# Optimization experiments

Hardware: AMD Instinct MI355X
Metric: run time of the kernel (lower is better)

Reference implementation:

```python
import jax, jax.numpy as jnp
import numpy as np

N_NODES = 100000
N_EDGES = 3200000
N_FEAT = 512
N_DIMS = 64
N_CLSS = 10


def setup_inputs() -> dict:
    key = jax.random.key(0)
    ks = jax.random.split(key, 8)
    x = jax.random.normal(ks[0], (N_NODES, N_FEAT), dtype=jnp.float32)
    edge_index = jax.random.randint(ks[1], (2, N_EDGES), 0, N_NODES, dtype=jnp.int64)
    edge_weight = jax.random.uniform(ks[2], (N_EDGES,), dtype=jnp.float32)
    W1 = jax.random.normal(ks[3], (N_FEAT, N_DIMS), dtype=jnp.float32) * (1.0 / np.sqrt(N_FEAT))
    M1 = jax.random.normal(ks[4], (N_FEAT, N_DIMS), dtype=jnp.float32)
    b1 = jnp.zeros((N_DIMS,), dtype=jnp.float32)
    W2 = jax.random.normal(ks[5], (N_DIMS, N_CLSS), dtype=jnp.float32) * (1.0 / np.sqrt(N_DIMS))
    M2 = jax.random.normal(ks[6], (N_DIMS, N_CLSS), dtype=jnp.float32)
    b2 = jnp.zeros((N_CLSS,), dtype=jnp.float32)
    return {"x": x, "edge_index": edge_index, "edge_weight": edge_weight,
            "W1": W1, "M1": M1, "b1": b1, "W2": W2, "M2": M2, "b2": b2}


def _gcn_conv(x, edge_index, edge_weight, W, M, b):
    # MaskedGCNConv: weight = W * mask, then standard GCN symmetric-normalized propagation.
    N = x.shape[0]
    h = x @ (W * M)  # [N, n_dims]  transform-first (in_feat > out_feat)
    # add self-loops with weight 1 (GCNConv default)
    loop = jnp.arange(N, dtype=edge_index.dtype)
    src = jnp.concatenate([edge_index[0], loop])
    dst = jnp.concatenate([edge_index[1], loop])
    w = jnp.concatenate([edge_weight, jnp.ones((N,), dtype=edge_weight.dtype)])
    deg = jax.ops.segment_sum(w, dst, num_segments=N)  # in-degree with weights
    deg_inv_sqrt = jnp.where(deg > 0, jax.lax.rsqrt(jnp.maximum(deg, 1e-12)), 0.0)
    norm = deg_inv_sqrt[src] * w * deg_inv_sqrt[dst]  # [E+N]
    out = jax.ops.segment_sum(h[src] * norm[:, None], dst, num_segments=N)
    return out + b


def reference(x, edge_index, edge_weight, W1, M1, b1, W2, M2, b2):
    h = jax.nn.relu(_gcn_conv(x, edge_index, edge_weight, W1, M1, b1))
    # F.dropout(training=self.training): identity in eval mode
    logits = h @ (W2 * M2) + b2  # MaskedLinear classifier
    return logits
```

## Files before the change

### kernel.cpp

```cpp
#include <hip/hip_runtime.h>

#define NN 100000
#define NE 3200000
#define NF 512
#define ND 64
#define NC 10
#define NB 391

#define OFF_H      0
#define OFF_RANK   0
#define OFF_DIS    6400000
#define OFF_W1     6500000
#define OFF_CNT    6533408
#define OFF_RP     6633408
#define OFF_BSUM   6733409
#define OFF_EDGE   6733922
#define OFF_W2F    13133922

typedef __attribute__((ext_vector_type(8))) short v8s;
typedef __attribute__((ext_vector_type(4))) float v4f;

__device__ __forceinline__ unsigned short bf16_rne(float f) {
  unsigned int u = __float_as_uint(f);
  return (unsigned short)((u + 0x7fffu + ((u >> 16) & 1u)) >> 16);
}

__global__ __launch_bounds__(256) void prep_kernel(
    const float* __restrict__ W1, const float* __restrict__ M1,
    const float* __restrict__ W2, const float* __restrict__ M2,
    float* __restrict__ ws) {
  const int i = blockIdx.x * 256 + threadIdx.x;
  if (i < NN) ((int*)ws)[OFF_CNT + i] = 0;
  if (i < NF * ND) {
    const float v = W1[i] * M1[i];
    const int k = i >> 6, d = i & 63;
    const int s = k >> 5, g = (k >> 3) & 3, e = k & 7;
    const int t = d >> 4;
    const int lane = (g << 4) | (d & 15);
    unsigned short* bp = (unsigned short*)(ws + OFF_W1);
    const int base = ((s * 4 + t) * 64 + lane) * 16 + e;
    const unsigned short hb = bf16_rne(v);
    bp[base] = hb;
    bp[base + 8] = bf16_rne(v - __uint_as_float((unsigned int)hb << 16));
  }
  if (i < ND * 16) {
    const int k = i >> 4, c = i & 15;
    const float v = (c < NC) ? W2[k * NC + c] * M2[k * NC + c] : 0.0f;
    const int s = k >> 5, g = (k >> 3) & 3, e = k & 7;
    const int lane = (g << 4) | c;
    unsigned short* bp = (unsigned short*)(ws + OFF_W2F);
    const int base = (s * 64 + lane) * 16 + e;
    const unsigned short hb = bf16_rne(v);
    bp[base] = hb;
    bp[base + 8] = bf16_rne(v - __uint_as_float((unsigned int)hb << 16));
  }
}

__global__ __launch_bounds__(256) void hist_kernel(
    const int* __restrict__ dst, int* __restrict__ cnt,
    int* __restrict__ rank) {
  const int e = blockIdx.x * 256 + threadIdx.x;
  rank[e] = atomicAdd(&cnt[dst[e]], 1);
}

__global__ __launch_bounds__(256) void scan_partial(
    const int* __restrict__ cnt, int* __restrict__ bsum) {
  __shared__ int s[256];
  const int i = blockIdx.x * 256 + threadIdx.x;
  int v = (i < NN) ? cnt[i] : 0;
  s[threadIdx.x] = v; __syncthreads();
  for (int off = 128; off > 0; off >>= 1) {
    if (threadIdx.x < off) s[threadIdx.x] += s[threadIdx.x + off];
    __syncthreads();
  }
  if (threadIdx.x == 0) bsum[blockIdx.x] = s[0];
}

__global__ __launch_bounds__(512) void scan_bsum(int* __restrict__ bsum) {
  __shared__ int s[512];
  const int t = threadIdx.x;
  const int v = (t < NB) ? bsum[t] : 0;
  s[t] = v; __syncthreads();
  for (int off = 1; off < 512; off <<= 1) {
    const int a = (t >= off) ? s[t - off] : 0;
    __syncthreads();
    s[t] += a;
    __syncthreads();
  }
  if (t < NB) bsum[t] = s[t] - v;
}

__global__ __launch_bounds__(256) void scan_final(
    const int* __restrict__ cnt, const int* __restrict__ bsum,
    int* __restrict__ rowptr) {
  __shared__ int s[256];
  const int i = blockIdx.x * 256 + threadIdx.x;
  const int v = (i < NN) ? cnt[i] : 0;
  s[threadIdx.x] = v; __syncthreads();
  for (int off = 1; off < 256; off <<= 1) {
    const int a = (threadIdx.x >= off) ? s[threadIdx.x - off] : 0;
    __syncthreads();
    s[threadIdx.x] += a;
    __syncthreads();
  }
  if (i < NN) {
    const int excl = s[threadIdx.x] - v + bsum[blockIdx.x];
    rowptr[i] = excl;
    if (i == NN - 1) rowptr[NN] = excl + v;
  }
}

__global__ __launch_bounds__(256) void fill_kernel(
    const int* __restrict__ src, const int* __restrict__ dst,
    const float* __restrict__ ew, const int* __restrict__ rank,
    const int* __restrict__ rowptr, int2* __restrict__ edge) {
  const int e = blockIdx.x * 256 + threadIdx.x;
  const int pos = rowptr[dst[e]] + rank[e];
  edge[pos] = make_int2(src[e], __float_as_int(ew[e]));
}

__global__ __launch_bounds__(256) void degdis_kernel(
    const int* __restrict__ rowptr, const int2* __restrict__ edge,
    float* __restrict__ dis) {
  const int n = blockIdx.x * 256 + threadIdx.x;
  if (n >= NN) return;
  const int beg = rowptr[n], end = rowptr[n + 1];
  float s = 1.0f;
  for (int e = beg; e < end; ++e) s += __int_as_float(edge[e].y);
  dis[n] = rsqrtf(s);
}

__global__ __launch_bounds__(256) void gemm1_kernel(
    const float* __restrict__ x, const float* __restrict__ bfrag_f,
    const float* __restrict__ dis, float* __restrict__ h) {
  const int lane = threadIdx.x & 63;
  const int wid  = threadIdx.x >> 6;
  const size_t row0 = ((size_t)blockIdx.x * 4 + wid) * 32;
  if (row0 >= NN) return;
  const int lr = lane & 15;
  const int lg = lane >> 4;
  const float* x0 = x + (row0 + lr) * NF + lg * 8;
  const v8s* bfr = (const v8s*)bfrag_f + (size_t)lane * 2;
  v4f acc[2][4];
#pragma unroll
  for (int i = 0; i < 2; ++i)
#pragma unroll
    for (int t = 0; t < 4; ++t) acc[i][t] = (v4f){0.f, 0.f, 0.f, 0.f};

  for (int s = 0; s < 16; ++s) {
    v8s ah[2], al[2];
#pragma unroll
    for (int i = 0; i < 2; ++i) {
      const float* xp = x0 + (size_t)i * (16 * NF) + s * 32;
      const float4 p0 = *(const float4*)xp;
      const float4 p1 = *(const float4*)(xp + 4);
      const float vv[8] = {p0.x, p0.y, p0.z, p0.w, p1.x, p1.y, p1.z, p1.w};
#pragma unroll
      for (int e = 0; e < 8; ++e) {
        const unsigned short hb = bf16_rne(vv[e]);
        ah[i][e] = (short)hb;
        al[i][e] = (short)bf16_rne(vv[e] - __uint_as_float((unsigned int)hb << 16));
      }
    }
#pragma unroll
    for (int t = 0; t < 4; ++t) {
      const v8s bh = bfr[(size_t)(s * 4 + t) * 128];
      const v8s bl = bfr[(size_t)(s * 4 + t) * 128 + 1];
#pragma unroll
      for (int i = 0; i < 2; ++i) {
        acc[i][t] = __builtin_amdgcn_mfma_f32_16x16x32_bf16(ah[i], bh, acc[i][t], 0, 0, 0);
        acc[i][t] = __builtin_amdgcn_mfma_f32_16x16x32_bf16(ah[i], bl, acc[i][t], 0, 0, 0);
        acc[i][t] = __builtin_amdgcn_mfma_f32_16x16x32_bf16(al[i], bh, acc[i][t], 0, 0, 0);
      }
    }
  }
#pragma unroll
  for (int i = 0; i < 2; ++i)
#pragma unroll
    for (int r = 0; r < 4; ++r) {
      const size_t row = row0 + i * 16 + lg * 4 + r;
      const float dv = dis[row];
#pragma unroll
      for (int t = 0; t < 4; ++t)
        h[row * ND + t * 16 + lr] = acc[i][t][r] * dv;
    }
}

__global__ __launch_bounds__(256) void gather_kernel(
    const int* __restrict__ rowptr, const int2* __restrict__ edge,
    const float* __restrict__ h, const float* __restrict__ dis,
    const float* __restrict__ b1, const float* __restrict__ w2f,
    const float* __restrict__ b2, float* __restrict__ out) {
  __shared__ float vls[4 * 64];
  const int lane = threadIdx.x & 63;
  const int wid  = threadIdx.x >> 6;
  const int n = blockIdx.x * 4 + wid;
  const int beg = __builtin_amdgcn_readfirstlane(rowptr[n]);
  const int end = __builtin_amdgcn_readfirstlane(rowptr[n + 1]);
  float a0 = 0.f, a1 = 0.f, a2 = 0.f, a3 = 0.f,
        a4 = 0.f, a5 = 0.f, a6 = 0.f, a7 = 0.f;
  int e = beg;
  for (; e + 8 <= end; e += 8) {
    const int2 q0 = edge[e],     q1 = edge[e + 1];
    const int2 q2 = edge[e + 2], q3 = edge[e + 3];
    const int2 q4 = edge[e + 4], q5 = edge[e + 5];
    const int2 q6 = edge[e + 6], q7 = edge[e + 7];
    a0 = fmaf(h[(size_t)q0.x * ND + lane], __int_as_float(q0.y), a0);
    a1 = fmaf(h[(size_t)q1.x * ND + lane], __int_as_float(q1.y), a1);
    a2 = fmaf(h[(size_t)q2.x * ND + lane], __int_as_float(q2.y), a2);
    a3 = fmaf(h[(size_t)q3.x * ND + lane], __int_as_float(q3.y), a3);
    a4 = fmaf(h[(size_t)q4.x * ND + lane], __int_as_float(q4.y), a4);
    a5 = fmaf(h[(size_t)q5.x * ND + lane], __int_as_float(q5.y), a5);
    a6 = fmaf(h[(size_t)q6.x * ND + lane], __int_as_float(q6.y), a6);
    a7 = fmaf(h[(size_t)q7.x * ND + lane], __int_as_float(q7.y), a7);
  }
  for (; e + 4 <= end; e += 4) {
    const int2 q0 = edge[e],     q1 = edge[e + 1];
    const int2 q2 = edge[e + 2], q3 = edge[e + 3];
    a0 = fmaf(h[(size_t)q0.x * ND + lane], __int_as_float(q0.y), a0);
    a1 = fmaf(h[(size_t)q1.x * ND + lane], __int_as_float(q1.y), a1);
    a2 = fmaf(h[(size_t)q2.x * ND + lane], __int_as_float(q2.y), a2);
    a3 = fmaf(h[(size_t)q3.x * ND + lane], __int_as_float(q3.y), a3);
  }
  for (; e < end; ++e) {
    const int2 q = edge[e];
    a0 = fmaf(h[(size_t)q.x * ND + lane], __int_as_float(q.y), a0);
  }
  const float dn = dis[n];
  const float hn = h[(size_t)n * ND + lane];
  float vv = fmaf((((a0 + a1) + (a2 + a3)) + ((a4 + a5) + (a6 + a7))) + hn,
                  dn, b1[lane]);
  vls[wid * 64 + lane] = fmaxf(vv, 0.0f);
  __syncthreads();
  if (wid == 0) {
    const int lr = lane & 15, lg = lane >> 4;
    const v8s* bfr = (const v8s*)w2f + (size_t)lane * 2;
    v4f acc = (v4f){0.f, 0.f, 0.f, 0.f};
#pragma unroll
    for (int s = 0; s < 2; ++s) {
      v8s ah, al;
#pragma unroll
      for (int k = 0; k < 8; ++k) {
        float xv = vls[(lr & 3) * 64 + s * 32 + lg * 8 + k];
        xv = (lr < 4) ? xv : 0.0f;
        const unsigned short hb = bf16_rne(xv);
        ah[k] = (short)hb;
        al[k] = (short)bf16_rne(xv - __uint_as_float((unsigned int)hb << 16));
      }
      const v8s bh = bfr[s * 128], bl = bfr[s * 128 + 1];
      acc = __builtin_amdgcn_mfma_f32_16x16x32_bf16(ah, bh, acc, 0, 0, 0);
      acc = __builtin_amdgcn_mfma_f32_16x16x32_bf16(ah, bl, acc, 0, 0, 0);
      acc = __builtin_amdgcn_mfma_f32_16x16x32_bf16(al, bh, acc, 0, 0, 0);
    }
    if (lane < NC) {
      const float bb = b2[lane];
#pragma unroll
      for (int r = 0; r < 4; ++r)
        out[(size_t)(blockIdx.x * 4 + r) * NC + lane] = acc[r] + bb;
    }
  }
}

extern "C" void kernel_launch(void* const* d_in, const int* in_sizes, int n_in,
                              void* d_out, int out_size, void* d_ws, size_t ws_size,
                              hipStream_t stream) {
  const float* x  = (const float*)d_in[0];
  const int*   ei = (const int*)d_in[1];
  const float* ew = (const float*)d_in[2];
  const float* W1 = (const float*)d_in[3];
  const float* M1 = (const float*)d_in[4];
  const float* b1 = (const float*)d_in[5];
  const float* W2 = (const float*)d_in[6];
  const float* M2 = (const float*)d_in[7];
  const float* b2 = (const float*)d_in[8];
  float* out = (float*)d_out;
  float* ws  = (float*)d_ws;
  int*   wsi = (int*)d_ws;
  const int* src = ei;
  const int* dst = ei + NE;
  int2* edge = (int2*)(wsi + OFF_EDGE);

  prep_kernel<<<NB, 256, 0, stream>>>(W1, M1, W2, M2, ws);
  hist_kernel<<<NE / 256, 256, 0, stream>>>(dst, wsi + OFF_CNT, wsi + OFF_RANK);
  scan_partial<<<NB, 256, 0, stream>>>(wsi + OFF_CNT, wsi + OFF_BSUM);
  scan_bsum<<<1, 512, 0, stream>>>(wsi + OFF_BSUM);
  scan_final<<<NB, 256, 0, stream>>>(wsi + OFF_CNT, wsi + OFF_BSUM, wsi + OFF_RP);
  fill_kernel<<<NE / 256, 256, 0, stream>>>(src, dst, ew, wsi + OFF_RANK,
                                            wsi + OFF_RP, edge);
  degdis_kernel<<<NB, 256, 0, stream>>>(wsi + OFF_RP, edge, ws + OFF_DIS);
  gemm1_kernel<<<(NN + 127) / 128, 256, 0, stream>>>(x, ws + OFF_W1,
                                                     ws + OFF_DIS, ws + OFF_H);
  gather_kernel<<<NN / 4, 256, 0, stream>>>(wsi + OFF_RP, edge, ws + OFF_H,
                                            ws + OFF_DIS, b1, ws + OFF_W2F, b2, out);
}
```

Baseline: 690.5 us.

## Replace global-atomic CSR build with two-level bucket partition sort

Replaces the per-edge global atomic histogram, rank array and scatter with a two-pass partitioned sort. Edges are first bucketed by coarse destination (512 nodes per bucket) using shared-memory histograms and cursors. Each bucket is then sorted locally in LDS, and the same pass computes rowptr and the degree rsqrt, which removes the separate degree kernel. This is meant to cut global atomic contention and random scatter traffic, at the cost of an extra pass over the edges through a temporary buffer placed in the H region.

```diff
diff --git a/kernel.cpp b/kernel.cpp
--- a/kernel.cpp
+++ b/kernel.cpp
@@ -5,13 +5,15 @@
 #define NF 512
 #define ND 64
 #define NC 10
-#define NB 391
+
+#define NBUCK 196
+#define NPB 500
+#define EPB 6400
 
 #define OFF_H      0
-#define OFF_RANK   0
 #define OFF_DIS    6400000
 #define OFF_W1     6500000
-#define OFF_CNT    6533408
+#define OFF_GH     6533408
 #define OFF_RP     6633408
 #define OFF_BSUM   6733409
 #define OFF_EDGE   6733922
@@ -30,7 +32,6 @@
     const float* __restrict__ W2, const float* __restrict__ M2,
     float* __restrict__ ws) {
   const int i = blockIdx.x * 256 + threadIdx.x;
-  if (i < NN) ((int*)ws)[OFF_CNT + i] = 0;
   if (i < NF * ND) {
     const float v = W1[i] * M1[i];
     const int k = i >> 6, d = i & 63;
@@ -56,30 +57,27 @@
   }
 }
 
-__global__ __launch_bounds__(256) void hist_kernel(
-    const int* __restrict__ dst, int* __restrict__ cnt,
-    int* __restrict__ rank) {
-  const int e = blockIdx.x * 256 + threadIdx.x;
-  rank[e] = atomicAdd(&cnt[dst[e]], 1);
-}
-
-__global__ __launch_bounds__(256) void scan_partial(
-    const int* __restrict__ cnt, int* __restrict__ bsum) {
-  __shared__ int s[256];
-  const int i = blockIdx.x * 256 + threadIdx.x;
-  int v = (i < NN) ? cnt[i] : 0;
-  s[threadIdx.x] = v; __syncthreads();
-  for (int off = 128; off > 0; off >>= 1) {
-    if (threadIdx.x < off) s[threadIdx.x] += s[threadIdx.x + off];
-    __syncthreads();
-  }
-  if (threadIdx.x == 0) bsum[blockIdx.x] = s[0];
-}
-
-__global__ __launch_bounds__(512) void scan_bsum(int* __restrict__ bsum) {
+
+__global__ __launch_bounds__(256) void part_hist(
+    const int* __restrict__ dst, int* __restrict__ GH) {
+  __shared__ int hist[NBUCK];
+  const int tid = threadIdx.x;
+  for (int i = tid; i < NBUCK; i += 256) hist[i] = 0;
+  __syncthreads();
+  const int s0 = blockIdx.x * EPB;
+  for (int e = s0 + tid; e < s0 + EPB; e += 256)
+    atomicAdd(&hist[dst[e] >> 9], 1);
+  __syncthreads();
+  for (int i = tid; i < NBUCK; i += 256)
+    GH[i * NPB + blockIdx.x] = hist[i];
+}
+
+__global__ __launch_bounds__(512) void part_scan(
+    int* __restrict__ GH, int* __restrict__ T) {
   __shared__ int s[512];
   const int t = threadIdx.x;
-  const int v = (t < NB) ? bsum[t] : 0;
+  const int b = blockIdx.x;
+  const int v = (t < NPB) ? GH[b * NPB + t] : 0;
   s[t] = v; __syncthreads();
   for (int off = 1; off < 512; off <<= 1) {
     const int a = (t >= off) ? s[t - off] : 0;
@@ -87,47 +85,85 @@
     s[t] += a;
     __syncthreads();
   }
-  if (t < NB) bsum[t] = s[t] - v;
-}
-
-__global__ __launch_bounds__(256) void scan_final(
-    const int* __restrict__ cnt, const int* __restrict__ bsum,
-    int* __restrict__ rowptr) {
+  if (t < NPB) GH[b * NPB + t] = s[t] - v;
+  if (t == 511) T[b] = s[511];
+}
+
+__global__ __launch_bounds__(256) void part_scan_t(
+    const int* __restrict__ T, int* __restrict__ TS) {
   __shared__ int s[256];
-  const int i = blockIdx.x * 256 + threadIdx.x;
-  const int v = (i < NN) ? cnt[i] : 0;
-  s[threadIdx.x] = v; __syncthreads();
+  const int t = threadIdx.x;
+  const int v = (t < NBUCK) ? T[t] : 0;
+  s[t] = v; __syncthreads();
   for (int off = 1; off < 256; off <<= 1) {
-    const int a = (threadIdx.x >= off) ? s[threadIdx.x - off] : 0;
-    __syncthreads();
-    s[threadIdx.x] += a;
-    __syncthreads();
-  }
-  if (i < NN) {
-    const int excl = s[threadIdx.x] - v + bsum[blockIdx.x];
-    rowptr[i] = excl;
-    if (i == NN - 1) rowptr[NN] = excl + v;
-  }
-}
-
-__global__ __launch_bounds__(256) void fill_kernel(
+    const int a = (t >= off) ? s[t - off] : 0;
+    __syncthreads();
+    s[t] += a;
+    __syncthreads();
+  }
+  if (t < NBUCK) TS[t] = s[t] - v;
+  if (t == NBUCK - 1) TS[NBUCK] = s[t];
+}
+
+__global__ __launch_bounds__(256) void part_scatter(
     const int* __restrict__ src, const int* __restrict__ dst,
-    const float* __restrict__ ew, const int* __restrict__ rank,
-    const int* __restrict__ rowptr, int2* __restrict__ edge) {
-  const int e = blockIdx.x * 256 + threadIdx.x;
-  const int pos = rowptr[dst[e]] + rank[e];
-  edge[pos] = make_int2(src[e], __float_as_int(ew[e]));
-}
-
-__global__ __launch_bounds__(256) void degdis_kernel(
-    const int* __restrict__ rowptr, const int2* __restrict__ edge,
+    const float* __restrict__ ew, const int* __restrict__ GH,
+    const int* __restrict__ TS, int2* __restrict__ buck) {
+  __shared__ int cursor[NBUCK];
+  const int tid = threadIdx.x;
+  for (int i = tid; i < NBUCK; i += 256)
+    cursor[i] = GH[i * NPB + blockIdx.x] + TS[i];
+  __syncthreads();
+  const int s0 = blockIdx.x * EPB;
+  for (int e = s0 + tid; e < s0 + EPB; e += 256) {
+    const int d = dst[e];
+    const int pos = atomicAdd(&cursor[d >> 9], 1);
+    buck[pos] = make_int2(src[e] | ((d & 511) << 17), __float_as_int(ew[e]));
+  }
+}
+
+__global__ __launch_bounds__(512) void bucket_sort(
+    const int* __restrict__ TS, const int2* __restrict__ buck,
+    int2* __restrict__ edge, int* __restrict__ rowptr,
     float* __restrict__ dis) {
-  const int n = blockIdx.x * 256 + threadIdx.x;
-  if (n >= NN) return;
-  const int beg = rowptr[n], end = rowptr[n + 1];
-  float s = 1.0f;
-  for (int e = beg; e < end; ++e) s += __int_as_float(edge[e].y);
-  dis[n] = rsqrtf(s);
+  __shared__ int hist[512];
+  __shared__ float deg[512];
+  __shared__ int scn[512];
+  const int t = threadIdx.x;
+  const int b = blockIdx.x;
+  const int beg = TS[b], endd = TS[b + 1];
+  hist[t] = 0; deg[t] = 0.0f;
+  __syncthreads();
+  for (int e = beg + t; e < endd; e += 512) {
+    const int2 q = buck[e];
+    const int fine = (q.x >> 17) & 511;
+    atomicAdd(&hist[fine], 1);
+    atomicAdd(&deg[fine], __int_as_float(q.y));
+  }
+  __syncthreads();
+  const int sv = hist[t];
+  scn[t] = sv; __syncthreads();
+  for (int off = 1; off < 512; off <<= 1) {
+    const int a = (t >= off) ? scn[t - off] : 0;
+    __syncthreads();
+    scn[t] += a;
+    __syncthreads();
+  }
+  const int ex = scn[t] - sv;
+  const int node = b * 512 + t;
+  if (node < NN) {
+    rowptr[node] = beg + ex;
+    dis[node] = rsqrtf(deg[t] + 1.0f);
+  }
+  if (b == NBUCK - 1 && t == 0) rowptr[NN] = endd;
+  hist[t] = beg + ex;
+  __syncthreads();
+  for (int e = beg + t; e < endd; e += 512) {
+    const int2 q = buck[e];
+    const int fine = (q.x >> 17) & 511;
+    const int pos = atomicAdd(&hist[fine], 1);
+    edge[pos] = make_int2(q.x & 0x1FFFF, q.y);
+  }
 }
 
 __global__ __launch_bounds__(256) void gemm1_kernel(
@@ -278,16 +314,19 @@
   int*   wsi = (int*)d_ws;
   const int* src = ei;
   const int* dst = ei + NE;
+  int2* buck = (int2*)(ws + OFF_H);
   int2* edge = (int2*)(wsi + OFF_EDGE);
-
-  prep_kernel<<<NB, 256, 0, stream>>>(W1, M1, W2, M2, ws);
-  hist_kernel<<<NE / 256, 256, 0, stream>>>(dst, wsi + OFF_CNT, wsi + OFF_RANK);
-  scan_partial<<<NB, 256, 0, stream>>>(wsi + OFF_CNT, wsi + OFF_BSUM);
-  scan_bsum<<<1, 512, 0, stream>>>(wsi + OFF_BSUM);
-  scan_final<<<NB, 256, 0, stream>>>(wsi + OFF_CNT, wsi + OFF_BSUM, wsi + OFF_RP);
-  fill_kernel<<<NE / 256, 256, 0, stream>>>(src, dst, ew, wsi + OFF_RANK,
-                                            wsi + OFF_RP, edge);
-  degdis_kernel<<<NB, 256, 0, stream>>>(wsi + OFF_RP, edge, ws + OFF_DIS);
+  int*  GH   = wsi + OFF_GH;
+  int*  T    = wsi + OFF_BSUM;
+  int*  TS   = wsi + OFF_BSUM + 256;
+
+  prep_kernel<<<128, 256, 0, stream>>>(W1, M1, W2, M2, ws);
+  part_hist<<<NPB, 256, 0, stream>>>(dst, GH);
+  part_scan<<<NBUCK, 512, 0, stream>>>(GH, T);
+  part_scan_t<<<1, 256, 0, stream>>>(T, TS);
+  part_scatter<<<NPB, 256, 0, stream>>>(src, dst, ew, GH, TS, buck);
+  bucket_sort<<<NBUCK, 512, 0, stream>>>(TS, buck, edge, wsi + OFF_RP,
+                                         ws + OFF_DIS);
   gemm1_kernel<<<(NN + 127) / 128, 256, 0, stream>>>(x, ws + OFF_W1,
                                                      ws + OFF_DIS, ws + OFF_H);
   gather_kernel<<<NN / 4, 256, 0, stream>>>(wsi + OFF_RP, edge, ws + OFF_H,
```

Measured after the change: 553.0 us. 1.25x faster.
